# Kernel tuning notes

Hardware: AMD Instinct MI355X
Metric: run time of the kernel (lower is better)

The kernel has to match this reference:

```python
import jax, jax.numpy as jnp
import numpy as np

VOCAB, DIM, H, T, B, OUT = 50000, 300, 100, 512, 256, 3

def setup_inputs() -> dict:
    key = jax.random.key(0)
    ks = jax.random.split(key, 20)
    s = 1.0 / np.sqrt(H)
    def u(k, shape):
        return jax.random.uniform(k, shape, jnp.float32, -s, s)
    inp = {
        'x': jax.random.randint(ks[0], (B, T), 0, VOCAB),
        'lengths': jnp.clip(jax.random.randint(ks[1], (B,), 0, T), 1, T),
        'emb': jax.random.normal(ks[2], (VOCAB, DIM), jnp.float32),
    }
    dims = [DIM, H, H]
    ki = 3
    for l in range(3):
        inp[f'w_ih{l}'] = u(ks[ki], (4 * H, dims[l])); ki += 1
        inp[f'w_hh{l}'] = u(ks[ki], (4 * H, H)); ki += 1
        inp[f'b_ih{l}'] = u(ks[ki], (4 * H,)); ki += 1
        inp[f'b_hh{l}'] = u(ks[ki], (4 * H,)); ki += 1
    inp['w_fc'] = u(ks[ki], (OUT, H)); ki += 1
    inp['b_fc'] = u(ks[ki], (OUT,))
    return inp

def _lstm_layer(inp, w_ih, w_hh, b_ih, b_hh, mask):
    # inp: [B,T,D], mask: [T,B,1] True where t < length
    xg = jnp.einsum('btd,gd->btg', inp, w_ih) + b_ih + b_hh  # [B,T,4H]
    h0 = jnp.zeros((inp.shape[0], H), inp.dtype)
    def step(carry, xs):
        h, c = carry
        xg_t, m = xs
        g = xg_t + h @ w_hh.T
        i, f, gg, o = jnp.split(g, 4, axis=-1)  # torch gate order i,f,g,o
        c_new = jax.nn.sigmoid(f) * c + jax.nn.sigmoid(i) * jnp.tanh(gg)
        h_new = jax.nn.sigmoid(o) * jnp.tanh(c_new)
        h = jnp.where(m, h_new, h)  # hold state past sequence end (packed-seq semantics)
        c = jnp.where(m, c_new, c)
        return (h, c), h
    (h_last, _), hs = jax.lax.scan(step, (h0, h0), (xg.transpose(1, 0, 2), mask))
    return hs.transpose(1, 0, 2), h_last

def reference(x, lengths, emb,
              w_ih0, w_hh0, b_ih0, b_hh0,
              w_ih1, w_hh1, b_ih1, b_hh1,
              w_ih2, w_hh2, b_ih2, b_hh2,
              w_fc, b_fc):
    e = emb[x]  # [B,T,DIM] embedding lookup (frozen table)
    mask = (jnp.arange(T)[:, None] < lengths[None, :])[:, :, None]  # [T,B,1]
    h = e
    params = [(w_ih0, w_hh0, b_ih0, b_hh0), (w_ih1, w_hh1, b_ih1, b_hh1), (w_ih2, w_hh2, b_ih2, b_hh2)]
    for (wi, wh, bi, bh) in params:
        h, h_last = _lstm_layer(h, wi, wh, bi, bh, mask)
    # dropout p=0.0 -> identity; final linear head
    return h_last @ w_fc.T + b_fc  # [B,OUT]
```

## Files before the change

kernel.cpp:

```cpp
#include <hip/hip_runtime.h>
#include <hip/hip_bf16.h>

#define T_STEPS 512
#define BATCH   256
#define HID     100
#define GATES   400
#define BT      (BATCH * T_STEPS)

__device__ __forceinline__ float sigm_f(float x) {
    return 1.f / (1.f + __expf(-x));
}

__device__ __forceinline__ float tanh_f(float x) {
    float ax = fabsf(x);
    float t  = __expf(-2.f * ax);
    float r  = (1.f - t) / (1.f + t);
    return copysignf(r, x);
}

__device__ __forceinline__ unsigned short bf_hi(float f) {
    unsigned u = __float_as_uint(f);
    return (unsigned short)((u + 0x7FFFu + ((u >> 16) & 1u)) >> 16);
}
__device__ __forceinline__ float bf_f(unsigned short s) {
    return __uint_as_float(((unsigned)s) << 16);
}

typedef short v8s __attribute__((ext_vector_type(8)));
typedef float v4f __attribute__((ext_vector_type(4)));

template <int K, int NK, bool GATHER>
__global__ __launch_bounds__(256) void xg_gemm(
    const float* __restrict__ A, const int* __restrict__ idx,
    const float* __restrict__ W, const float* __restrict__ b1,
    const float* __restrict__ b2, float* __restrict__ out)
{
    __shared__ unsigned short Ah[2][4096], Al[2][4096];
    __shared__ unsigned short Wh[2][4096], Wl[2][4096];
    __shared__ int idx_s[128];

    const int bid  = blockIdx.x;
    const int xcd  = bid & 7;
    const int rest = bid >> 3;
    const int ct   = rest & 3;
    const int rgrp = rest >> 2;
    const int row0 = (rgrp * 8 + xcd) * 128;
    const int col0 = ct * 128;

    const int tid  = threadIdx.x;
    const int lane = tid & 63;
    const int wave = tid >> 6;
    const int wm   = wave >> 1;
    const int wn   = wave & 1;
    const int lm   = lane & 15;
    const int lk   = lane >> 4;

    if (GATHER) {
        if (tid < 128) idx_s[tid] = idx[row0 + tid];
        __syncthreads();
    }

    const int sr = tid >> 1;
    const int sq = (tid & 1) * 4;
    const float* arowp = GATHER ? (A + (size_t)idx_s[sr] * K)
                                : (A + (size_t)(row0 + sr) * K);
    const int    wrow  = col0 + sr;
    const bool   wval  = (wrow < GATES);
    const float* wrowp = W + (size_t)wrow * K;

    auto stage = [&](int ks, int buf) {
        const int k0 = ks * 32;
#pragma unroll
        for (int u = 0; u < 4; ++u) {
            int q  = sq + u;
            int kb = k0 + q * 4;
            float4 va = make_float4(0.f, 0.f, 0.f, 0.f);
            float4 vw = make_float4(0.f, 0.f, 0.f, 0.f);
            if (kb < K) {
                va = *(const float4*)(arowp + kb);
                if (wval) vw = *(const float4*)(wrowp + kb);
            }
            int bo = sr * 64 + q * 8;
            int so = bo ^ (((bo >> 6) & 7) << 4);
            unsigned short h0 = bf_hi(va.x), h1 = bf_hi(va.y),
                           h2 = bf_hi(va.z), h3 = bf_hi(va.w);
            *(ushort4*)((char*)Ah[buf] + so) = make_ushort4(h0, h1, h2, h3);
            *(ushort4*)((char*)Al[buf] + so) = make_ushort4(
                bf_hi(va.x - bf_f(h0)), bf_hi(va.y - bf_f(h1)),
                bf_hi(va.z - bf_f(h2)), bf_hi(va.w - bf_f(h3)));
            h0 = bf_hi(vw.x); h1 = bf_hi(vw.y);
            h2 = bf_hi(vw.z); h3 = bf_hi(vw.w);
            *(ushort4*)((char*)Wh[buf] + so) = make_ushort4(h0, h1, h2, h3);
            *(ushort4*)((char*)Wl[buf] + so) = make_ushort4(
                bf_hi(vw.x - bf_f(h0)), bf_hi(vw.y - bf_f(h1)),
                bf_hi(vw.z - bf_f(h2)), bf_hi(vw.w - bf_f(h3)));
        }
    };

    stage(0, 0);

    v4f acc[4][4];
#pragma unroll
    for (int fm = 0; fm < 4; ++fm)
#pragma unroll
        for (int fn = 0; fn < 4; ++fn)
            acc[fm][fn] = (v4f){0.f, 0.f, 0.f, 0.f};

#pragma unroll 1
    for (int ks = 0; ks < NK; ++ks) {
        __syncthreads();
        if (ks + 1 < NK) stage(ks + 1, (ks + 1) & 1);

        const int cur = ks & 1;
        v8s ah[4], al[4], bh[4], bl[4];
#pragma unroll
        for (int f = 0; f < 4; ++f) {
            int ra = (wm * 64 + f * 16 + lm) * 64 + lk * 16;
            ra ^= ((ra >> 6) & 7) << 4;
            ah[f] = *(const v8s*)((const char*)Ah[cur] + ra);
            al[f] = *(const v8s*)((const char*)Al[cur] + ra);
            int rb = (wn * 64 + f * 16 + lm) * 64 + lk * 16;
            rb ^= ((rb >> 6) & 7) << 4;
            bh[f] = *(const v8s*)((const char*)Wh[cur] + rb);
            bl[f] = *(const v8s*)((const char*)Wl[cur] + rb);
        }
#pragma unroll
        for (int fm = 0; fm < 4; ++fm) {
#pragma unroll
            for (int fn = 0; fn < 4; ++fn) {
                acc[fm][fn] = __builtin_amdgcn_mfma_f32_16x16x32_bf16(
                    ah[fm], bh[fn], acc[fm][fn], 0, 0, 0);
                acc[fm][fn] = __builtin_amdgcn_mfma_f32_16x16x32_bf16(
                    ah[fm], bl[fn], acc[fm][fn], 0, 0, 0);
                acc[fm][fn] = __builtin_amdgcn_mfma_f32_16x16x32_bf16(
                    al[fm], bh[fn], acc[fm][fn], 0, 0, 0);
            }
        }
    }

#pragma unroll
    for (int fn = 0; fn < 4; ++fn) {
        int col = col0 + wn * 64 + fn * 16 + lm;
        if (col < GATES) {
            float bias = b1[col] + b2[col];
#pragma unroll
            for (int fm = 0; fm < 4; ++fm) {
                v4f d = acc[fm][fn];
                int rbase = row0 + wm * 64 + fm * 16 + lk * 4;
#pragma unroll
                for (int p = 0; p < 4; ++p)
                    out[(size_t)(rbase + p) * GATES + col] = d[p] + bias;
            }
        }
    }
}

#define LOADW(W0, W1, W2, W3, W4, W5, W6, P)                 \
    W0 = (v4f){(P)[0],  (P)[1],  (P)[2],  (P)[3]};           \
    W1 = (v4f){(P)[4],  (P)[5],  (P)[6],  (P)[7]};           \
    W2 = (v4f){(P)[8],  (P)[9],  (P)[10], (P)[11]};          \
    W3 = (v4f){(P)[12], (P)[13], (P)[14], (P)[15]};          \
    W4 = (v4f){(P)[16], (P)[17], (P)[18], (P)[19]};          \
    W5 = (v4f){(P)[20], (P)[21], (P)[22], (P)[23]};          \
    W6 = (v4f){(P)[24], 0.f, 0.f, 0.f};

#define DOT4(S, W, H)                                        \
    S += (W).x * (H).x; S += (W).y * (H).y;                  \
    S += (W).z * (H).z; S += (W).w * (H).w;

template <bool WRITE_ALL>
__global__ __launch_bounds__(448, 2) void lstm_recur(
    const float* __restrict__ xg,
    const float* __restrict__ w_hh,
    const int*   __restrict__ lengths,
    float* __restrict__ hs)
{
    const int b   = blockIdx.x;
    const int tid = threadIdx.x;
    const bool active = (tid < 400);
    const int j   = tid >> 2;
    const int jc  = (j < HID) ? j : (HID - 1);
    const int gt  = tid & 3;

    __shared__ float xg_s[32 * GATES];
    __shared__ float h_s[2][112];
    __shared__ float h_hist[32 * HID];

    v4f w00, w01, w02, w03, w04, w05, w06;
    v4f w10, w11, w12, w13, w14, w15, w16;
    v4f w20, w21, w22, w23, w24, w25, w26;
    v4f w30, w31, w32, w33, w34, w35, w36;
    {
        const float* p0 = w_hh + (size_t)(0 * HID + jc) * HID + gt * 25;
        const float* p1 = w_hh + (size_t)(1 * HID + jc) * HID + gt * 25;
        const float* p2 = w_hh + (size_t)(2 * HID + jc) * HID + gt * 25;
        const float* p3 = w_hh + (size_t)(3 * HID + jc) * HID + gt * 25;
        LOADW(w00, w01, w02, w03, w04, w05, w06, p0)
        LOADW(w10, w11, w12, w13, w14, w15, w16, p1)
        LOADW(w20, w21, w22, w23, w24, w25, w26, p2)
        LOADW(w30, w31, w32, w33, w34, w35, w36, p3)
    }

    for (int i = tid; i < 224; i += 448) ((float*)h_s)[i] = 0.f;

    float c_reg = 0.f, h_reg = 0.f;
    const int len = lengths[b];
    const float* xgb = xg + (size_t)b * T_STEPS * GATES;
    float*       hsb = hs + (size_t)b * T_STEPS * HID;

    const bool is0 = (gt == 0), is1 = (gt == 1), is2 = (gt == 2);
    const int  hoff = gt * 28;
    const int  seg  = (jc / 25) * 28 + (jc % 25);
    const int  xcol = gt * HID + jc;

    for (int t = 0; t < T_STEPS; ++t) {
        if ((t & 31) == 0) {
            if (WRITE_ALL && t > 0) {
                const float4* s = (const float4*)h_hist;
                float4*       d = (float4*)(hsb + (size_t)(t - 32) * HID);
                for (int i = tid; i < 800; i += 448) d[i] = s[i];
            }
            const float4* src = (const float4*)(xgb + (size_t)t * GATES);
            float4*       dst = (float4*)xg_s;
            for (int i = tid; i < 3200; i += 448) dst[i] = src[i];
            __syncthreads();
        }

        asm volatile("" : "+v"(w00), "+v"(w01), "+v"(w02), "+v"(w03),
                          "+v"(w04), "+v"(w05), "+v"(w06));
        asm volatile("" : "+v"(w10), "+v"(w11), "+v"(w12), "+v"(w13),
                          "+v"(w14), "+v"(w15), "+v"(w16));
        asm volatile("" : "+v"(w20), "+v"(w21), "+v"(w22), "+v"(w23),
                          "+v"(w24), "+v"(w25), "+v"(w26));
        asm volatile("" : "+v"(w30), "+v"(w31), "+v"(w32), "+v"(w33),
                          "+v"(w34), "+v"(w35), "+v"(w36));

        float s0 = 0.f, s1 = 0.f, s2 = 0.f, s3 = 0.f;
        {
            const v4f* hb = (const v4f*)(h_s[t & 1] + hoff);
            v4f ha = hb[0], hb1 = hb[1], hc = hb[2], hd = hb[3],
                he = hb[4], hf = hb[5], hg = hb[6];
            DOT4(s0, w00, ha) DOT4(s0, w01, hb1) DOT4(s0, w02, hc)
            DOT4(s0, w03, hd) DOT4(s0, w04, he)  DOT4(s0, w05, hf)
            DOT4(s0, w06, hg)
            DOT4(s1, w10, ha) DOT4(s1, w11, hb1) DOT4(s1, w12, hc)
            DOT4(s1, w13, hd) DOT4(s1, w14, he)  DOT4(s1, w15, hf)
            DOT4(s1, w16, hg)
            DOT4(s2, w20, ha) DOT4(s2, w21, hb1) DOT4(s2, w22, hc)
            DOT4(s2, w23, hd) DOT4(s2, w24, he)  DOT4(s2, w25, hf)
            DOT4(s2, w26, hg)
            DOT4(s3, w30, ha) DOT4(s3, w31, hb1) DOT4(s3, w32, hc)
            DOT4(s3, w33, hd) DOT4(s3, w34, he)  DOT4(s3, w35, hf)
            DOT4(s3, w36, hg)
        }
        s0 += __shfl_xor(s0, 1); s0 += __shfl_xor(s0, 2);
        s1 += __shfl_xor(s1, 1); s1 += __shfl_xor(s1, 2);
        s2 += __shfl_xor(s2, 1); s2 += __shfl_xor(s2, 2);
        s3 += __shfl_xor(s3, 1); s3 += __shfl_xor(s3, 2);

        float sg  = is0 ? s0 : is1 ? s1 : is2 ? s2 : s3;
        float pre = sg + xg_s[(t & 31) * GATES + xcol];

        float p0 = is2 ? tanh_f(pre) : sigm_f(pre);
        float p1 = __shfl_xor(p0, 1);
        float p2 = __shfl_xor(p0, 2);
        float p3 = __shfl_xor(p1, 2);
        float iv = is0 ? p0 : is1 ? p1 : is2 ? p2 : p3;
        float fv = is0 ? p1 : is1 ? p0 : is2 ? p3 : p2;
        float gv = is0 ? p2 : is1 ? p3 : is2 ? p0 : p1;
        float ov = is0 ? p3 : is1 ? p2 : is2 ? p1 : p0;

        float c_new = fv * c_reg + iv * gv;
        float h_new = ov * tanh_f(c_new);
        bool  m     = (t < len);
        c_reg = m ? c_new : c_reg;
        h_reg = m ? h_new : h_reg;

        if (active && gt == 0) {
            h_s[(t & 1) ^ 1][seg] = h_reg;
            if (WRITE_ALL) h_hist[(t & 31) * HID + j] = h_reg;
        }
        __syncthreads();
    }

    if (WRITE_ALL) {
        const float4* s = (const float4*)h_hist;
        float4*       d = (float4*)(hsb + (size_t)(T_STEPS - 32) * HID);
        for (int i = tid; i < 800; i += 448) d[i] = s[i];
    } else {
        if (active && gt == 0)
            hsb[(size_t)(T_STEPS - 1) * HID + j] = h_reg;
    }
}

__global__ __launch_bounds__(64) void fc_kernel(
    const float* __restrict__ hs, const float* __restrict__ w_fc,
    const float* __restrict__ b_fc, float* __restrict__ out)
{
    int tid = blockIdx.x * 64 + threadIdx.x;
    if (tid >= BATCH * 3) return;
    int b = tid / 3, o = tid % 3;
    const float* h = hs + ((size_t)b * T_STEPS + (T_STEPS - 1)) * HID;
    float acc = b_fc[o];
    for (int j = 0; j < HID; ++j) acc += h[j] * w_fc[o * HID + j];
    out[b * 3 + o] = acc;
}

extern "C" void kernel_launch(void* const* d_in, const int* in_sizes, int n_in,
                              void* d_out, int out_size, void* d_ws, size_t ws_size,
                              hipStream_t stream)
{
    const int*   x       = (const int*)  d_in[0];
    const int*   lengths = (const int*)  d_in[1];
    const float* emb     = (const float*)d_in[2];
    const float* w_ih0   = (const float*)d_in[3];
    const float* w_hh0   = (const float*)d_in[4];
    const float* b_ih0   = (const float*)d_in[5];
    const float* b_hh0   = (const float*)d_in[6];
    const float* w_ih1   = (const float*)d_in[7];
    const float* w_hh1   = (const float*)d_in[8];
    const float* b_ih1   = (const float*)d_in[9];
    const float* b_hh1   = (const float*)d_in[10];
    const float* w_ih2   = (const float*)d_in[11];
    const float* w_hh2   = (const float*)d_in[12];
    const float* b_ih2   = (const float*)d_in[13];
    const float* b_hh2   = (const float*)d_in[14];
    const float* w_fc    = (const float*)d_in[15];
    const float* b_fc    = (const float*)d_in[16];
    float* out = (float*)d_out;

    float* xg = (float*)d_ws;
    float* hs = xg + (size_t)BT * GATES;

    const int nblk = (BT / 128) * 4;

    xg_gemm<300, 10, true><<<nblk, 256, 0, stream>>>(emb, x, w_ih0, b_ih0, b_hh0, xg);
    lstm_recur<true><<<BATCH, 448, 0, stream>>>(xg, w_hh0, lengths, hs);

    xg_gemm<100, 4, false><<<nblk, 256, 0, stream>>>(hs, nullptr, w_ih1, b_ih1, b_hh1, xg);
    lstm_recur<true><<<BATCH, 448, 0, stream>>>(xg, w_hh1, lengths, hs);

    xg_gemm<100, 4, false><<<nblk, 256, 0, stream>>>(hs, nullptr, w_ih2, b_ih2, b_hh2, xg);
    lstm_recur<false><<<BATCH, 448, 0, stream>>>(xg, w_hh2, lengths, hs);

    fc_kernel<<<(BATCH * 3 + 63) / 64, 64, 0, stream>>>(hs, w_fc, b_fc, out);
}
```

Measured before the change: 1.984 ms.

## Skip padded timesteps in input-gate GEMM and LSTM recurrence

```diff
diff --git a/kernel.cpp b/kernel.cpp
--- a/kernel.cpp
+++ b/kernel.cpp
@@ -33,7 +33,8 @@
 __global__ __launch_bounds__(256) void xg_gemm(
     const float* __restrict__ A, const int* __restrict__ idx,
     const float* __restrict__ W, const float* __restrict__ b1,
-    const float* __restrict__ b2, float* __restrict__ out)
+    const float* __restrict__ b2, const int* __restrict__ lengths,
+    float* __restrict__ out)
 {
     __shared__ unsigned short Ah[2][4096], Al[2][4096];
     __shared__ unsigned short Wh[2][4096], Wl[2][4096];
@@ -46,6 +47,8 @@
     const int rgrp = rest >> 2;
     const int row0 = (rgrp * 8 + xcd) * 128;
     const int col0 = ct * 128;
+
+    if ((row0 & 511) >= lengths[row0 >> 9]) return;
 
     const int tid  = threadIdx.x;
     const int lane = tid & 63;
@@ -169,7 +172,7 @@
     S += (W).z * (H).z; S += (W).w * (H).w;
 
 template <bool WRITE_ALL>
-__global__ __launch_bounds__(448, 2) void lstm_recur(
+__global__ __launch_bounds__(448) void lstm_recur(
     const float* __restrict__ xg,
     const float* __restrict__ w_hh,
     const int*   __restrict__ lengths,
@@ -204,7 +207,8 @@
     for (int i = tid; i < 224; i += 448) ((float*)h_s)[i] = 0.f;
 
     float c_reg = 0.f, h_reg = 0.f;
-    const int len = lengths[b];
+    const int len   = lengths[b];
+    const int t_end = (len + 31) & ~31;
     const float* xgb = xg + (size_t)b * T_STEPS * GATES;
     float*       hsb = hs + (size_t)b * T_STEPS * HID;
 
@@ -213,7 +217,7 @@
     const int  seg  = (jc / 25) * 28 + (jc % 25);
     const int  xcol = gt * HID + jc;
 
-    for (int t = 0; t < T_STEPS; ++t) {
+    for (int t = 0; t < t_end; ++t) {
         if ((t & 31) == 0) {
             if (WRITE_ALL && t > 0) {
                 const float4* s = (const float4*)h_hist;
@@ -225,15 +229,6 @@
             for (int i = tid; i < 3200; i += 448) dst[i] = src[i];
             __syncthreads();
         }
-
-        asm volatile("" : "+v"(w00), "+v"(w01), "+v"(w02), "+v"(w03),
-                          "+v"(w04), "+v"(w05), "+v"(w06));
-        asm volatile("" : "+v"(w10), "+v"(w11), "+v"(w12), "+v"(w13),
-                          "+v"(w14), "+v"(w15), "+v"(w16));
-        asm volatile("" : "+v"(w20), "+v"(w21), "+v"(w22), "+v"(w23),
-                          "+v"(w24), "+v"(w25), "+v"(w26));
-        asm volatile("" : "+v"(w30), "+v"(w31), "+v"(w32), "+v"(w33),
-                          "+v"(w34), "+v"(w35), "+v"(w36));
 
         float s0 = 0.f, s1 = 0.f, s2 = 0.f, s3 = 0.f;
         {
@@ -284,9 +279,16 @@
     }
 
     if (WRITE_ALL) {
-        const float4* s = (const float4*)h_hist;
-        float4*       d = (float4*)(hsb + (size_t)(T_STEPS - 32) * HID);
-        for (int i = tid; i < 800; i += 448) d[i] = s[i];
+        {
+            const float4* s = (const float4*)h_hist;
+            float4*       d = (float4*)(hsb + (size_t)(t_end - 32) * HID);
+            for (int i = tid; i < 800; i += 448) d[i] = s[i];
+        }
+        const float* hfin = h_s[t_end & 1];
+        for (int e = tid; e < (T_STEPS - t_end) * HID; e += 448) {
+            int t = t_end + e / HID, jj = e % HID;
+            hsb[(size_t)t * HID + jj] = hfin[(jj / 25) * 28 + (jj % 25)];
+        }
     } else {
         if (active && gt == 0)
             hsb[(size_t)(T_STEPS - 1) * HID + j] = h_reg;
@@ -334,13 +336,13 @@
 
     const int nblk = (BT / 128) * 4;
 
-    xg_gemm<300, 10, true><<<nblk, 256, 0, stream>>>(emb, x, w_ih0, b_ih0, b_hh0, xg);
+    xg_gemm<300, 10, true><<<nblk, 256, 0, stream>>>(emb, x, w_ih0, b_ih0, b_hh0, lengths, xg);
     lstm_recur<true><<<BATCH, 448, 0, stream>>>(xg, w_hh0, lengths, hs);
 
-    xg_gemm<100, 4, false><<<nblk, 256, 0, stream>>>(hs, nullptr, w_ih1, b_ih1, b_hh1, xg);
+    xg_gemm<100, 4, false><<<nblk, 256, 0, stream>>>(hs, nullptr, w_ih1, b_ih1, b_hh1, lengths, xg);
     lstm_recur<true><<<BATCH, 448, 0, stream>>>(xg, w_hh1, lengths, hs);
 
-    xg_gemm<100, 4, false><<<nblk, 256, 0, stream>>>(hs, nullptr, w_ih2, b_ih2, b_hh2, xg);
+    xg_gemm<100, 4, false><<<nblk, 256, 0, stream>>>(hs, nullptr, w_ih2, b_ih2, b_hh2, lengths, xg);
     lstm_recur<false><<<BATCH, 448, 0, stream>>>(xg, w_hh2, lengths, hs);
 
     fc_kernel<<<(BATCH * 3 + 63) / 64, 64, 0, stream>>>(hs, w_fc, b_fc, out);
```

Measured after the change: 1.873 ms. 1.06x faster.
